# Kernel optimization log

Hardware: AMD Instinct MI355X
Metric: run time of the kernel (lower is better)

The kernel has to match this reference:

```python
import jax, jax.numpy as jnp
import numpy as np

T, B, D, H = 512, 256, 256, 512


def setup_inputs() -> dict:
    key = jax.random.key(0)
    k1, k2, k3, k4 = jax.random.split(key, 4)
    x = jax.random.normal(k1, (T, B, D), dtype=jnp.float32)
    hidden_state = jnp.zeros((1, B, H), dtype=jnp.float32)
    episode_starts = jax.random.randint(k2, (T, B), 0, 2, dtype=jnp.int32)
    # PyTorch GRU params, gate order (r, z, n); xavier-ish / orthogonal-ish scale via randn*scale
    w_ih = jax.random.normal(k3, (3 * H, D), dtype=jnp.float32) * (1.0 / np.sqrt(D))
    w_hh = jax.random.normal(k4, (3 * H, H), dtype=jnp.float32) * (1.0 / np.sqrt(H))
    b_ih = jnp.zeros((3 * H,), dtype=jnp.float32)
    b_hh = jnp.zeros((3 * H,), dtype=jnp.float32)
    return {"x": x, "hidden_state": hidden_state, "episode_starts": episode_starts,
            "w_ih": w_ih, "w_hh": w_hh, "b_ih": b_ih, "b_hh": b_hh}


def _gru_scan(x, h0, episode_starts, w_ih, w_hh, b_ih, b_hh):
    # Precompute input projections for all timesteps: [T, B, 3H]
    gi_all = jnp.einsum('tbd,gd->tbg', x, w_ih) + b_ih
    keep_all = 1.0 - (episode_starts != 0).astype(x.dtype)  # [T, B]
    hsz = h0.shape[-1]

    def step(h, inputs):
        gi, keep = inputs          # gi: [B, 3H], keep: [B]
        h = h * keep[:, None]      # episode reset
        gh = h @ w_hh.T + b_hh     # [B, 3H]
        gi_r, gi_z, gi_n = gi[:, :hsz], gi[:, hsz:2 * hsz], gi[:, 2 * hsz:]
        gh_r, gh_z, gh_n = gh[:, :hsz], gh[:, hsz:2 * hsz], gh[:, 2 * hsz:]
        r = jax.nn.sigmoid(gi_r + gh_r)
        z = jax.nn.sigmoid(gi_z + gh_z)
        n = jnp.tanh(gi_n + r * gh_n)
        h_new = (1.0 - z) * n + z * h
        return h_new, h_new

    h_final, outputs = jax.lax.scan(step, h0, (gi_all, keep_all))
    return outputs, h_final


def reference(x, hidden_state, episode_starts, w_ih, w_hh, b_ih, b_hh):
    h0 = hidden_state[0]  # num_layers=1 -> [B, H]
    outputs, h_final = _gru_scan(x, h0, episode_starts, w_ih, w_hh, b_ih, b_hh)
    return outputs, h_final[None]  # ([T, B, H], [1, B, H])
```

## Files before the change

kernel.cpp:

```cpp
#include <hip/hip_runtime.h>
#include <stdint.h>

#define TT 512
#define BB 256
#define DD 256
#define HH 512

#define WSL 32
#define NGROUP 16
#define KS_X 8
#define KS_H 16
#define KS_TOT 24
#define NBLK 144

typedef __attribute__((ext_vector_type(8))) short short8;
typedef __attribute__((ext_vector_type(4))) float floatx4;

__device__ __forceinline__ short f2bf(float v) {
    union { float f; uint32_t u; } x; x.f = v;
    uint32_t r = (x.u + 0x7fffu + ((x.u >> 16) & 1u)) >> 16;
    return (short)r;
}
__device__ __forceinline__ float bf2f(unsigned int s) {
    union { uint32_t u; float f; } x; x.u = (s & 0xffffu) << 16;
    return x.f;
}
__device__ __forceinline__ float sigm(float v) { return 1.0f / (1.0f + __expf(-v)); }

__global__ void init_flags(unsigned int* f) { f[threadIdx.x * 32] = 0u; }

__global__ __launch_bounds__(128, 1)
void gru_persistent(const float* __restrict__ x,
                    const float* __restrict__ h0,
                    const int*   __restrict__ ep,
                    const float* __restrict__ w_ih,
                    const float* __restrict__ w_hh,
                    const float* __restrict__ b_ih,
                    const float* __restrict__ b_hh,
                    float* __restrict__ out,
                    unsigned int* __restrict__ flags,
                    unsigned short* __restrict__ exch) {
    __shared__ short ldsw[NBLK * 512];

    const int tid  = threadIdx.x;
    const int lane = tid & 63;
    const int w    = tid >> 6;
    const int b    = blockIdx.x;
    const int xcd = b & 7;
    const int idx = b >> 3;
    const int bg  = xcd * 2 + (idx >> 4);
    const int sl  = idx & 15;

    for (int u = tid; u < NBLK * 64; u += 128) {
        int blk = u >> 6;
        int l   = u & 63;
        int ww  = blk / 72;
        int rem = blk % 72;
        int g   = rem / 24;
        int ks  = rem % 24;
        int row = sl * WSL + ww * 16 + (l & 15) + g * HH;
        int k0  = ks * 32 + ((l >> 4) * 8);
        const float* src = (k0 < DD) ? (w_ih + (size_t)row * DD + k0)
                                     : (w_hh + (size_t)row * HH + (k0 - DD));
        short8 v;
        #pragma unroll
        for (int j = 0; j < 8; j++) v[j] = f2bf(src[j]);
        *(short8*)&ldsw[(size_t)blk * 512 + l * 8] = v;
    }
    __syncthreads();

    const int cl   = lane & 15;
    const int col  = sl * WSL + w * 16 + cl;
    const int am   = bg * 16 + cl;
    const int rbase = (lane >> 4) * 4;
    const int k0a  = (lane >> 4) * 8;
    const float br0 = b_ih[col] + b_hh[col];
    const float bz0 = b_ih[col + HH] + b_hh[col + HH];
    const float bin = b_ih[col + 2 * HH];
    const float bhn = b_hh[col + 2 * HH];

    for (int t = 0; t < TT; t++) {
        floatx4 accI[3], accH[3];
        #pragma unroll
        for (int g = 0; g < 3; g++) {
            accI[g] = (floatx4){0.f, 0.f, 0.f, 0.f};
            accH[g] = (floatx4){0.f, 0.f, 0.f, 0.f};
        }

        const float* xrow = x + ((size_t)t * BB + am) * DD;
        #pragma unroll
        for (int ks = 0; ks < KS_X; ks++) {
            int k0 = ks * 32 + k0a;
            short8 a;
            #pragma unroll
            for (int j = 0; j < 8; j++) a[j] = f2bf(xrow[k0 + j]);
            #pragma unroll
            for (int g = 0; g < 3; g++) {
                short8 bf = *(const short8*)&ldsw[(size_t)((w * 3 + g) * KS_TOT + ks) * 512 + lane * 8];
                accI[g] = __builtin_amdgcn_mfma_f32_16x16x32_bf16(a, bf, accI[g], 0, 0, 0);
            }
        }
        const float keepA = (ep[t * BB + am] != 0) ? 0.0f : 1.0f;

        if (t > 0) {
            if (w == 0) {
                const unsigned int target = (unsigned int)t;
                for (;;) {
                    unsigned int v = 0xFFFFFFFFu;
                    if (lane < NGROUP)
                        v = __hip_atomic_load(&flags[(bg * NGROUP + lane) * 32],
                                              __ATOMIC_RELAXED, __HIP_MEMORY_SCOPE_AGENT);
                    if (__all(v >= target)) break;
                    __builtin_amdgcn_s_sleep(1);
                }
            }
            __syncthreads();
        }

        const unsigned short* hbuf = exch + ((size_t)((t & 1) ^ 1)) * BB * HH;
        short8 a[KS_H];
        unsigned int hp[4];
        if (t == 0) {
            const float* hrow = h0 + (size_t)am * HH;
            #pragma unroll
            for (int ks = 0; ks < KS_H; ks++) {
                int k0 = ks * 32 + k0a;
                #pragma unroll
                for (int j = 0; j < 8; j++) a[ks][j] = f2bf(hrow[k0 + j] * keepA);
            }
        } else {
            const unsigned short* hb = hbuf + (size_t)am * HH + k0a;
            #pragma unroll
            for (int ks = 0; ks < KS_H; ks++) {
                asm volatile("global_load_dwordx4 %0, %1, off sc0 sc1"
                             : "=&v"(a[ks]) : "v"(hb + ks * 32) : "memory");
            }
            #pragma unroll
            for (int j = 0; j < 4; j++) {
                const unsigned short* hq = hbuf + (size_t)(bg * 16 + rbase + j) * HH + col;
                asm volatile("global_load_ushort %0, %1, off sc0 sc1"
                             : "=&v"(hp[j]) : "v"(hq) : "memory");
            }
            asm volatile("s_waitcnt vmcnt(0)" ::: "memory");
            __builtin_amdgcn_sched_barrier(0);
            if (keepA == 0.0f) {
                #pragma unroll
                for (int ks = 0; ks < KS_H; ks++) a[ks] = (short8)0;
            }
        }

        #pragma unroll
        for (int ks = 0; ks < KS_H; ks++) {
            #pragma unroll
            for (int g = 0; g < 3; g++) {
                short8 bf = *(const short8*)&ldsw[(size_t)((w * 3 + g) * KS_TOT + KS_X + ks) * 512 + lane * 8];
                accH[g] = __builtin_amdgcn_mfma_f32_16x16x32_bf16(a[ks], bf, accH[g], 0, 0, 0);
            }
        }

        unsigned short* exw = exch + ((size_t)(t & 1)) * BB * HH;
        float hnv[4];
        #pragma unroll
        for (int j = 0; j < 4; j++) {
            const int mo = bg * 16 + rbase + j;
            const float keep = (ep[t * BB + mo] != 0) ? 0.0f : 1.0f;
            float hprev;
            if (t == 0) hprev = h0[(size_t)mo * HH + col] * keep;
            else        hprev = bf2f(hp[j]) * keep;
            const float r = sigm(accI[0][j] + accH[0][j] + br0);
            const float z = sigm(accI[1][j] + accH[1][j] + bz0);
            const float n = tanhf(accI[2][j] + bin + r * (accH[2][j] + bhn));
            hnv[j] = (1.0f - z) * n + z * hprev;
            if (t < TT - 1) {
                unsigned short* pw = exw + (size_t)mo * HH + col;
                unsigned int bits = (unsigned int)(unsigned short)f2bf(hnv[j]);
                asm volatile("global_store_short %0, %1, off sc0 sc1"
                             :: "v"(pw), "v"(bits) : "memory");
            }
        }

        if (t < TT - 1) {
            asm volatile("s_waitcnt vmcnt(0)" ::: "memory");
            __syncthreads();
            if (tid == 0) {
                __hip_atomic_store(&flags[(bg * NGROUP + sl) * 32], (unsigned int)(t + 1),
                                   __ATOMIC_RELAXED, __HIP_MEMORY_SCOPE_AGENT);
            }
        }

        #pragma unroll
        for (int j = 0; j < 4; j++) {
            const int mo = bg * 16 + rbase + j;
            out[((size_t)t * BB + mo) * HH + col] = hnv[j];
            if (t == TT - 1) out[(size_t)TT * BB * HH + (size_t)mo * HH + col] = hnv[j];
        }
    }
}

extern "C" void kernel_launch(void* const* d_in, const int* in_sizes, int n_in,
                              void* d_out, int out_size, void* d_ws, size_t ws_size,
                              hipStream_t stream) {
    const float* x   = (const float*)d_in[0];
    const float* h0  = (const float*)d_in[1];
    const int*   ep  = (const int*)d_in[2];
    const float* wih = (const float*)d_in[3];
    const float* whh = (const float*)d_in[4];
    const float* bih = (const float*)d_in[5];
    const float* bhh = (const float*)d_in[6];
    float* out = (float*)d_out;

    unsigned int*   flags = (unsigned int*)d_ws;
    unsigned short* exch  = (unsigned short*)((char*)d_ws + 32768);

    hipLaunchKernelGGL(init_flags, dim3(1), dim3(256), 0, stream, flags);
    hipLaunchKernelGGL(gru_persistent, dim3(256), dim3(128), 0, stream,
                       x, h0, ep, wih, whh, bih, bhh, out, flags, exch);
}
```

Measured before the change: 3.288 ms.

## Replace flag barrier with timestep-tagged hidden-state words polled directly

```diff
diff --git a/kernel.cpp b/kernel.cpp
--- a/kernel.cpp
+++ b/kernel.cpp
@@ -15,19 +15,24 @@
 
 typedef __attribute__((ext_vector_type(8))) short short8;
 typedef __attribute__((ext_vector_type(4))) float floatx4;
+typedef __attribute__((ext_vector_type(4))) unsigned int uintx4;
 
 __device__ __forceinline__ short f2bf(float v) {
     union { float f; uint32_t u; } x; x.f = v;
     uint32_t r = (x.u + 0x7fffu + ((x.u >> 16) & 1u)) >> 16;
     return (short)r;
 }
-__device__ __forceinline__ float bf2f(unsigned int s) {
-    union { uint32_t u; float f; } x; x.u = (s & 0xffffu) << 16;
+__device__ __forceinline__ float bf2f_hi(unsigned int s) {
+    union { uint32_t u; float f; } x; x.u = s & 0xffff0000u;
     return x.f;
 }
 __device__ __forceinline__ float sigm(float v) { return 1.0f / (1.0f + __expf(-v)); }
 
-__global__ void init_flags(unsigned int* f) { f[threadIdx.x * 32] = 0u; }
+__global__ __launch_bounds__(256)
+void clear_exch(unsigned int* e) {
+    uintx4 v = {0xFFFFFFFFu, 0xFFFFFFFFu, 0xFFFFFFFFu, 0xFFFFFFFFu};
+    *(uintx4*)(e + ((size_t)blockIdx.x * 256 + threadIdx.x) * 4) = v;
+}
 
 __global__ __launch_bounds__(128, 1)
 void gru_persistent(const float* __restrict__ x,
@@ -38,8 +43,7 @@
                     const float* __restrict__ b_ih,
                     const float* __restrict__ b_hh,
                     float* __restrict__ out,
-                    unsigned int* __restrict__ flags,
-                    unsigned short* __restrict__ exch) {
+                    unsigned int* __restrict__ exch) {
     __shared__ short ldsw[NBLK * 512];
 
     const int tid  = threadIdx.x;
@@ -102,24 +106,8 @@
         }
         const float keepA = (ep[t * BB + am] != 0) ? 0.0f : 1.0f;
 
-        if (t > 0) {
-            if (w == 0) {
-                const unsigned int target = (unsigned int)t;
-                for (;;) {
-                    unsigned int v = 0xFFFFFFFFu;
-                    if (lane < NGROUP)
-                        v = __hip_atomic_load(&flags[(bg * NGROUP + lane) * 32],
-                                              __ATOMIC_RELAXED, __HIP_MEMORY_SCOPE_AGENT);
-                    if (__all(v >= target)) break;
-                    __builtin_amdgcn_s_sleep(1);
-                }
-            }
-            __syncthreads();
-        }
-
-        const unsigned short* hbuf = exch + ((size_t)((t & 1) ^ 1)) * BB * HH;
         short8 a[KS_H];
-        unsigned int hp[4];
+        float hprev_raw[4];
         if (t == 0) {
             const float* hrow = h0 + (size_t)am * HH;
             #pragma unroll
@@ -128,25 +116,63 @@
                 #pragma unroll
                 for (int j = 0; j < 8; j++) a[ks][j] = f2bf(hrow[k0 + j] * keepA);
             }
+            #pragma unroll
+            for (int j = 0; j < 4; j++)
+                hprev_raw[j] = h0[(size_t)(bg * 16 + rbase + j) * HH + col];
         } else {
-            const unsigned short* hb = hbuf + (size_t)am * HH + k0a;
+            const unsigned int tgt = (unsigned int)(t - 1);
+            const unsigned int* exr = exch + ((size_t)((t & 1) ^ 1)) * BB * HH;
+            const unsigned int* hb  = exr + (size_t)am * HH + k0a;
+            const unsigned int* hq0 = exr + (size_t)(bg * 16 + rbase) * HH + col;
+            const unsigned int* hq2 = exr + (size_t)(bg * 16 + rbase + 2) * HH + col;
+            uintx4 u0[KS_H], u1[KS_H];
+            unsigned int hp[4];
+            for (;;) {
+                #pragma unroll
+                for (int ks = 0; ks < KS_H; ks++) {
+                    asm volatile("global_load_dwordx4 %0, %2, off offset:%c3 sc0 sc1\n\t"
+                                 "global_load_dwordx4 %1, %2, off offset:%c4 sc0 sc1"
+                                 : "=&v"(u0[ks]), "=&v"(u1[ks])
+                                 : "v"(hb), "n"(ks * 128), "n"(ks * 128 + 16)
+                                 : "memory");
+                }
+                asm volatile("global_load_dword %0, %2, off sc0 sc1\n\t"
+                             "global_load_dword %1, %2, off offset:2048 sc0 sc1"
+                             : "=&v"(hp[0]), "=&v"(hp[1]) : "v"(hq0) : "memory");
+                asm volatile("global_load_dword %0, %2, off sc0 sc1\n\t"
+                             "global_load_dword %1, %2, off offset:2048 sc0 sc1"
+                             : "=&v"(hp[2]), "=&v"(hp[3]) : "v"(hq2) : "memory");
+                asm volatile("s_waitcnt vmcnt(0)" ::: "memory");
+                __builtin_amdgcn_sched_barrier(0);
+                unsigned int bad = 0;
+                #pragma unroll
+                for (int ks = 0; ks < KS_H; ks++) {
+                    #pragma unroll
+                    for (int j = 0; j < 4; j++) {
+                        bad |= (u0[ks][j] ^ tgt) & 0xffffu;
+                        bad |= (u1[ks][j] ^ tgt) & 0xffffu;
+                    }
+                }
+                #pragma unroll
+                for (int j = 0; j < 4; j++) bad |= (hp[j] ^ tgt) & 0xffffu;
+                if (__all(bad == 0)) break;
+                __builtin_amdgcn_s_sleep(1);
+            }
             #pragma unroll
             for (int ks = 0; ks < KS_H; ks++) {
-                asm volatile("global_load_dwordx4 %0, %1, off sc0 sc1"
-                             : "=&v"(a[ks]) : "v"(hb + ks * 32) : "memory");
-            }
-            #pragma unroll
-            for (int j = 0; j < 4; j++) {
-                const unsigned short* hq = hbuf + (size_t)(bg * 16 + rbase + j) * HH + col;
-                asm volatile("global_load_ushort %0, %1, off sc0 sc1"
-                             : "=&v"(hp[j]) : "v"(hq) : "memory");
-            }
-            asm volatile("s_waitcnt vmcnt(0)" ::: "memory");
-            __builtin_amdgcn_sched_barrier(0);
+                union { short8 s; uintx4 u; } cv;
+                cv.u[0] = (u0[ks][1] & 0xffff0000u) | (u0[ks][0] >> 16);
+                cv.u[1] = (u0[ks][3] & 0xffff0000u) | (u0[ks][2] >> 16);
+                cv.u[2] = (u1[ks][1] & 0xffff0000u) | (u1[ks][0] >> 16);
+                cv.u[3] = (u1[ks][3] & 0xffff0000u) | (u1[ks][2] >> 16);
+                a[ks] = cv.s;
+            }
             if (keepA == 0.0f) {
                 #pragma unroll
                 for (int ks = 0; ks < KS_H; ks++) a[ks] = (short8)0;
             }
+            #pragma unroll
+            for (int j = 0; j < 4; j++) hprev_raw[j] = bf2f_hi(hp[j]);
         }
 
         #pragma unroll
@@ -158,33 +184,23 @@
             }
         }
 
-        unsigned short* exw = exch + ((size_t)(t & 1)) * BB * HH;
+        unsigned int* exw = exch + ((size_t)(t & 1)) * BB * HH;
         float hnv[4];
         #pragma unroll
         for (int j = 0; j < 4; j++) {
             const int mo = bg * 16 + rbase + j;
             const float keep = (ep[t * BB + mo] != 0) ? 0.0f : 1.0f;
-            float hprev;
-            if (t == 0) hprev = h0[(size_t)mo * HH + col] * keep;
-            else        hprev = bf2f(hp[j]) * keep;
+            const float hprev = hprev_raw[j] * keep;
             const float r = sigm(accI[0][j] + accH[0][j] + br0);
             const float z = sigm(accI[1][j] + accH[1][j] + bz0);
             const float n = tanhf(accI[2][j] + bin + r * (accH[2][j] + bhn));
             hnv[j] = (1.0f - z) * n + z * hprev;
             if (t < TT - 1) {
-                unsigned short* pw = exw + (size_t)mo * HH + col;
-                unsigned int bits = (unsigned int)(unsigned short)f2bf(hnv[j]);
-                asm volatile("global_store_short %0, %1, off sc0 sc1"
-                             :: "v"(pw), "v"(bits) : "memory");
-            }
-        }
-
-        if (t < TT - 1) {
-            asm volatile("s_waitcnt vmcnt(0)" ::: "memory");
-            __syncthreads();
-            if (tid == 0) {
-                __hip_atomic_store(&flags[(bg * NGROUP + sl) * 32], (unsigned int)(t + 1),
-                                   __ATOMIC_RELAXED, __HIP_MEMORY_SCOPE_AGENT);
+                unsigned int* pw = exw + (size_t)mo * HH + col;
+                unsigned int word = (((unsigned int)(unsigned short)f2bf(hnv[j])) << 16)
+                                  | (unsigned int)(t & 0xffff);
+                asm volatile("global_store_dword %0, %1, off sc0 sc1"
+                             :: "v"(pw), "v"(word) : "memory");
             }
         }
 
@@ -209,10 +225,9 @@
     const float* bhh = (const float*)d_in[6];
     float* out = (float*)d_out;
 
-    unsigned int*   flags = (unsigned int*)d_ws;
-    unsigned short* exch  = (unsigned short*)((char*)d_ws + 32768);
-
-    hipLaunchKernelGGL(init_flags, dim3(1), dim3(256), 0, stream, flags);
+    unsigned int* exch = (unsigned int*)d_ws;
+
+    hipLaunchKernelGGL(clear_exch, dim3(256), dim3(256), 0, stream, exch);
     hipLaunchKernelGGL(gru_persistent, dim3(256), dim3(128), 0, stream,
-                       x, h0, ep, wih, whh, bih, bhh, out, flags, exch);
-}
+                       x, h0, ep, wih, whh, bih, bhh, out, exch);
+}
```

New measurement: 3.299 ms. About the same (+0.3%).
